# Optimization experiments

Hardware: AMD Instinct MI355X
Metric: run time of the kernel (lower is better)

The kernel has to match this reference:

```python
import jax, jax.numpy as jnp
import numpy as np

N_NODES = 200000
N_EDGES = 2000000
N_GRAPHS = 10000
N_LAYERS = 2
BN_EPS = 1e-5


def setup_inputs() -> dict:
    key = jax.random.key(0)
    ks = jax.random.split(key, 24)
    inp = {
        "x": jax.random.normal(ks[0], (N_NODES, 14), dtype=jnp.float32),
        "edge_index": jax.random.randint(ks[1], (2, N_EDGES), 0, N_NODES, dtype=jnp.int32),
        "edge_attr": jax.random.normal(ks[2], (N_EDGES, 3), dtype=jnp.float32),
        "batch": jnp.sort(jax.random.randint(ks[3], (N_NODES,), 0, N_GRAPHS, dtype=jnp.int32)),
        # embeddings
        "node_w": jax.random.normal(ks[4], (14, 32), dtype=jnp.float32) * 0.2,
        "node_b": jnp.zeros((32,), dtype=jnp.float32),
        "edge_w": jax.random.normal(ks[5], (3, 32), dtype=jnp.float32) * 0.2,
        "edge_b": jnp.zeros((32,), dtype=jnp.float32),
        # per-layer GINE MLP (32->75->32) + BatchNorm params, stacked over layers
        "w1": jax.random.normal(ks[6], (N_LAYERS, 32, 75), dtype=jnp.float32) * 0.15,
        "b1": jnp.zeros((N_LAYERS, 75), dtype=jnp.float32),
        "w2": jax.random.normal(ks[7], (N_LAYERS, 75, 32), dtype=jnp.float32) * 0.15,
        "b2": jnp.zeros((N_LAYERS, 32), dtype=jnp.float32),
        "bn_g": jnp.ones((N_LAYERS, 32), dtype=jnp.float32),
        "bn_b": jnp.zeros((N_LAYERS, 32), dtype=jnp.float32),
        # readout head
        "lin1_w": jax.random.normal(ks[8], (32, 16), dtype=jnp.float32) * 0.2,
        "lin1_b": jnp.zeros((16,), dtype=jnp.float32),
        "lin2_w": jax.random.normal(ks[9], (16, 2), dtype=jnp.float32) * 0.2,
        "lin2_b": jnp.zeros((2,), dtype=jnp.float32),
    }
    return inp


def reference(x, edge_index, edge_attr, batch,
              node_w, node_b, edge_w, edge_b,
              w1, b1, w2, b2, bn_g, bn_b,
              lin1_w, lin1_b, lin2_w, lin2_b):
    n = x.shape[0]
    src, dst = edge_index[0], edge_index[1]
    h = x @ node_w + node_b                      # [N,32]
    e = edge_attr @ edge_w + edge_b              # [E,32]
    for l in range(N_LAYERS):
        # GINEConv: (1+eps)*x + sum_j ReLU(x_j + e_ij), eps=0, then MLP
        msg = jax.nn.relu(h[src] + e)            # [E,32] gather + edge add
        agg = jax.ops.segment_sum(msg, dst, num_segments=n)  # scatter-sum
        z = h + agg
        z = jax.nn.relu(z @ w1[l] + b1[l]) @ w2[l] + b2[l]
        # BatchNorm (training-mode batch statistics, biased var)
        mu = jnp.mean(z, axis=0)
        var = jnp.var(z, axis=0)
        z = (z - mu) * jax.lax.rsqrt(var + BN_EPS) * bn_g[l] + bn_b[l]
        h = jax.nn.relu(z)
    # global mean pool over graphs
    counts = jax.ops.segment_sum(jnp.ones((n,), dtype=h.dtype), batch, num_segments=N_GRAPHS)
    g = jax.ops.segment_sum(h, batch, num_segments=N_GRAPHS) / jnp.maximum(counts, 1.0)[:, None]
    pred = jax.nn.relu(g @ lin1_w + lin1_b) @ lin2_w + lin2_b  # [G,2] logits
    return pred
```

## Files before the change

kernel.cpp:

```cpp
#include <hip/hip_runtime.h>
#include <hip/hip_fp16.h>

#define NN 200000
#define NE 2000000
#define NG 10000

#define NPB 256
#define NBKT 782
#define EPB 8192
#define NPBLK 245
#define SCAN_N (NBKT * NPBLK)
#define SCAN_PAD 191592
#define NSB1 ((SCAN_N + 255) / 256)

typedef __fp16 h2 __attribute__((ext_vector_type(2)));

__device__ __forceinline__ void fadd(float* p, float v) {
    unsafeAtomicAdd(p, v);
}

__device__ __forceinline__ float fdot2(h2 a, h2 b, float c) {
#if __has_builtin(__builtin_amdgcn_fdot2)
    return __builtin_amdgcn_fdot2(a, b, c, false);
#else
    return c + (float)a.x * (float)b.x + (float)a.y * (float)b.y;
#endif
}

__device__ __forceinline__ h2 pk16(float a, float b) {
#if __has_builtin(__builtin_amdgcn_cvt_pkrtz)
    return __builtin_amdgcn_cvt_pkrtz(a, b);
#else
    h2 r;
    r.x = (__fp16)a;
    r.y = (__fp16)b;
    return r;
#endif
}

__device__ __forceinline__ float4 h16_load4(const __half* p) {
    uint2 r = *reinterpret_cast<const uint2*>(p);
    __half2 a = *reinterpret_cast<__half2*>(&r.x);
    __half2 b = *reinterpret_cast<__half2*>(&r.y);
    float2 f0 = __half22float2(a);
    float2 f1 = __half22float2(b);
    return make_float4(f0.x, f0.y, f1.x, f1.y);
}

__device__ __forceinline__ void h16_store4(__half* p, float4 v) {
    __half2 a = __floats2half2_rn(v.x, v.y);
    __half2 b = __floats2half2_rn(v.z, v.w);
    uint2 r;
    r.x = *reinterpret_cast<uint*>(&a);
    r.y = *reinterpret_cast<uint*>(&b);
    *reinterpret_cast<uint2*>(p) = r;
}

__global__ __launch_bounds__(256) void k_node_embed(const float* __restrict__ x,
                                                    const float* __restrict__ w,
                                                    const float* __restrict__ b,
                                                    __half* __restrict__ h16) {
    __shared__ float sw[14 * 32];
    __shared__ float sb[32];
    for (int i = threadIdx.x; i < 14 * 32; i += 256) sw[i] = w[i];
    if (threadIdx.x < 32) sb[threadIdx.x] = b[threadIdx.x];
    __syncthreads();
    int n = blockIdx.x * 256 + threadIdx.x;
    if (n >= NN) return;
    float xi[14];
#pragma unroll
    for (int k = 0; k < 14; ++k) xi[k] = x[n * 14 + k];
#pragma unroll
    for (int c = 0; c < 32; c += 4) {
        float4 acc = make_float4(sb[c], sb[c + 1], sb[c + 2], sb[c + 3]);
#pragma unroll
        for (int k = 0; k < 14; ++k) {
            float xv = xi[k];
            acc.x += xv * sw[k * 32 + c + 0];
            acc.y += xv * sw[k * 32 + c + 1];
            acc.z += xv * sw[k * 32 + c + 2];
            acc.w += xv * sw[k * 32 + c + 3];
        }
        h16_store4(h16 + (size_t)n * 32 + c, acc);
    }
}

__global__ __launch_bounds__(256) void k_prep(const float* __restrict__ w1,
                                              const float* __restrict__ b1,
                                              const float* __restrict__ w2,
                                              uint* __restrict__ w1h,
                                              uint* __restrict__ w2p,
                                              float* __restrict__ b1p) {
    int i = blockIdx.x * 256 + threadIdx.x;
    if (i < 2 * 76 * 16) {
        int l = i / (76 * 16), r = i % (76 * 16);
        int j = r / 16, p = r % 16;
        float a = (j < 75) ? w1[l * 2400 + (2 * p) * 75 + j] : 0.f;
        float b = (j < 75) ? w1[l * 2400 + (2 * p + 1) * 75 + j] : 0.f;
        uint lo = __half_as_ushort(__float2half_rn(a));
        uint hi = __half_as_ushort(__float2half_rn(b));
        w1h[i] = lo | (hi << 16);
        return;
    }
    int i2 = i - 2 * 76 * 16;
    if (i2 >= 0 && i2 < 2 * 38 * 32) {
        int l = i2 / (38 * 32), r = i2 % (38 * 32);
        int jp = r / 32, k = r % 32;
        float a = w2[l * 2400 + (2 * jp) * 32 + k];
        float b = (2 * jp + 1 < 75) ? w2[l * 2400 + (2 * jp + 1) * 32 + k] : 0.f;
        uint lo = __half_as_ushort(__float2half_rn(a));
        uint hi = __half_as_ushort(__float2half_rn(b));
        w2p[i2] = lo | (hi << 16);
        return;
    }
    int i3 = i2 - 2 * 38 * 32;
    if (i3 >= 0 && i3 < 2 * 76) {
        int l = i3 / 76, j = i3 % 76;
        b1p[i3] = (j < 75) ? b1[l * 75 + j] : 0.f;
    }
}

__global__ __launch_bounds__(1024) void k_hist(const int* __restrict__ ei,
                                               int* __restrict__ counts) {
    __shared__ int hist[NBKT];
    for (int i = threadIdx.x; i < NBKT; i += 1024) hist[i] = 0;
    __syncthreads();
    int base = blockIdx.x * EPB;
#pragma unroll
    for (int k = 0; k < EPB / 1024; ++k) {
        int e = base + k * 1024 + threadIdx.x;
        if (e < NE) atomicAdd(&hist[ei[NE + e] >> 8], 1);
    }
    __syncthreads();
    for (int b = threadIdx.x; b < NBKT; b += 1024)
        counts[b * NPBLK + blockIdx.x] = hist[b];
}

__global__ __launch_bounds__(256) void k_scanA(int* __restrict__ data,
                                               int* __restrict__ part) {
    __shared__ int s[256];
    int tid = threadIdx.x;
    int i = blockIdx.x * 256 + tid;
    int v = (i < SCAN_N) ? data[i] : 0;
    s[tid] = v;
    __syncthreads();
    for (int off = 1; off < 256; off <<= 1) {
        int t = (tid >= off) ? s[tid - off] : 0;
        __syncthreads();
        s[tid] += t;
        __syncthreads();
    }
    if (i < SCAN_N) data[i] = s[tid] - v;
    if (tid == 255) part[blockIdx.x] = s[255];
}

__global__ __launch_bounds__(1024) void k_scanB(int* __restrict__ part) {
    __shared__ int s[1024];
    int tid = threadIdx.x;
    int v = (tid < NSB1) ? part[tid] : 0;
    s[tid] = v;
    __syncthreads();
    for (int off = 1; off < 1024; off <<= 1) {
        int t = (tid >= off) ? s[tid - off] : 0;
        __syncthreads();
        s[tid] += t;
        __syncthreads();
    }
    if (tid < NSB1) part[tid] = s[tid] - v;
}

__global__ __launch_bounds__(256) void k_scanC(int* __restrict__ data,
                                               const int* __restrict__ part) {
    int i = blockIdx.x * 256 + threadIdx.x;
    if (i < SCAN_N) data[i] += part[blockIdx.x];
}

__global__ __launch_bounds__(1024) void k_part_scatter(const int* __restrict__ ei,
                                                       const float* __restrict__ ea,
                                                       const int* __restrict__ counts,
                                                       uint3* __restrict__ tmp) {
    __shared__ int sbase[NBKT];
    __shared__ int scnt[NBKT];
    for (int i = threadIdx.x; i < NBKT; i += 1024) {
        sbase[i] = counts[i * NPBLK + blockIdx.x];
        scnt[i] = 0;
    }
    __syncthreads();
    int base = blockIdx.x * EPB;
#pragma unroll
    for (int k = 0; k < EPB / 1024; ++k) {
        int e = base + k * 1024 + threadIdx.x;
        if (e >= NE) continue;
        int dst = ei[NE + e];
        int bkt = dst >> 8;
        int nl = dst & 255;
        int r = atomicAdd(&scnt[bkt], 1);
        int src = ei[e];
        __half2 p01 = __floats2half2_rn(ea[e * 3 + 0], ea[e * 3 + 1]);
        __half p2 = __float2half_rn(ea[e * 3 + 2]);
        uint3 rec;
        rec.x = (uint)(src | (nl << 24));
        rec.y = *reinterpret_cast<const uint*>(&p01);
        rec.z = (uint)__half_as_ushort(p2);
        tmp[sbase[bkt] + r] = rec;
    }
}

__global__ __launch_bounds__(512) void k_bucket_sort(const int* __restrict__ counts,
                                                     const uint3* __restrict__ tmp,
                                                     uint3* __restrict__ recs2,
                                                     int* __restrict__ row_off) {
    __shared__ int cnt[NPB];
    __shared__ int s[NPB];
    int tid = threadIdx.x;
    int b = blockIdx.x;
    int boff = counts[b * NPBLK];
    int bend = (b == NBKT - 1) ? NE : counts[(b + 1) * NPBLK];
    if (tid < NPB) cnt[tid] = 0;
    __syncthreads();
    for (int i = boff + tid; i < bend; i += 512)
        atomicAdd(&cnt[(tmp[i].x >> 24) & 255], 1);
    __syncthreads();
    int v = (tid < NPB) ? cnt[tid] : 0;
    if (tid < NPB) s[tid] = v;
    __syncthreads();
    for (int off = 1; off < 256; off <<= 1) {
        int t = (tid >= off && tid < NPB) ? s[tid - off] : 0;
        __syncthreads();
        if (tid < NPB) s[tid] += t;
        __syncthreads();
    }
    if (tid < NPB) {
        int excl = s[tid] - v;
        int n = b * NPB + tid;
        if (n < NN) row_off[n] = boff + excl;
        cnt[tid] = excl;
    }
    if (b == NBKT - 1 && tid == 0) row_off[NN] = NE;
    __syncthreads();
    for (int i = boff + tid; i < bend; i += 512) {
        uint3 r = tmp[i];
        int nl = (r.x >> 24) & 255;
        int p = atomicAdd(&cnt[nl], 1);
        recs2[boff + p] = r;
    }
}

__global__ __launch_bounds__(256) void k_aggregate(const int* __restrict__ row_off,
                                                   const uint3* __restrict__ recs,
                                                   const float* __restrict__ ew,
                                                   const float* __restrict__ eb,
                                                   const __half* __restrict__ h16,
                                                   float* __restrict__ agg) {
    __shared__ float sw[96];
    __shared__ float sb[32];
    if (threadIdx.x < 96) sw[threadIdx.x] = ew[threadIdx.x];
    if (threadIdx.x < 32) sb[threadIdx.x] = eb[threadIdx.x];
    __syncthreads();
    int t = blockIdx.x * 256 + threadIdx.x;
    int n = t >> 2;
    if (n >= NN) return;
    int c = (t & 3) * 8;
    float w0[8], w1[8], w2[8], bb[8], acc[8];
#pragma unroll
    for (int j = 0; j < 8; ++j) {
        w0[j] = sw[c + j];
        w1[j] = sw[32 + c + j];
        w2[j] = sw[64 + c + j];
        bb[j] = sb[c + j];
        acc[j] = 0.f;
    }
    int s0 = row_off[n], s1 = row_off[n + 1];
    int i = s0;
    for (; i + 2 <= s1; i += 2) {
        uint3 r0 = recs[i];
        uint3 r1 = recs[i + 1];
        int src0 = r0.x & 0x00FFFFFF;
        int src1 = r1.x & 0x00FFFFFF;
        uint4 ha = *(const uint4*)(h16 + (size_t)src0 * 32 + c);
        uint4 hb = *(const uint4*)(h16 + (size_t)src1 * 32 + c);
        float2 e01a = __half22float2(*reinterpret_cast<const __half2*>(&r0.y));
        float e2a = __half2float(__ushort_as_half((unsigned short)(r0.z & 0xFFFF)));
        float2 e01b = __half22float2(*reinterpret_cast<const __half2*>(&r1.y));
        float e2b = __half2float(__ushort_as_half((unsigned short)(r1.z & 0xFFFF)));
        float fa[8], fb[8];
        {
            float2 t0 = __half22float2(*reinterpret_cast<const __half2*>(&ha.x));
            float2 t1 = __half22float2(*reinterpret_cast<const __half2*>(&ha.y));
            float2 t2 = __half22float2(*reinterpret_cast<const __half2*>(&ha.z));
            float2 t3 = __half22float2(*reinterpret_cast<const __half2*>(&ha.w));
            fa[0] = t0.x; fa[1] = t0.y; fa[2] = t1.x; fa[3] = t1.y;
            fa[4] = t2.x; fa[5] = t2.y; fa[6] = t3.x; fa[7] = t3.y;
            float2 u0 = __half22float2(*reinterpret_cast<const __half2*>(&hb.x));
            float2 u1 = __half22float2(*reinterpret_cast<const __half2*>(&hb.y));
            float2 u2 = __half22float2(*reinterpret_cast<const __half2*>(&hb.z));
            float2 u3 = __half22float2(*reinterpret_cast<const __half2*>(&hb.w));
            fb[0] = u0.x; fb[1] = u0.y; fb[2] = u1.x; fb[3] = u1.y;
            fb[4] = u2.x; fb[5] = u2.y; fb[6] = u3.x; fb[7] = u3.y;
        }
#pragma unroll
        for (int j = 0; j < 8; ++j) {
            float ma = fa[j] + bb[j] + e01a.x * w0[j] + e01a.y * w1[j] + e2a * w2[j];
            float mb = fb[j] + bb[j] + e01b.x * w0[j] + e01b.y * w1[j] + e2b * w2[j];
            acc[j] += fmaxf(ma, 0.f) + fmaxf(mb, 0.f);
        }
    }
    if (i < s1) {
        uint3 r0 = recs[i];
        int src0 = r0.x & 0x00FFFFFF;
        uint4 ha = *(const uint4*)(h16 + (size_t)src0 * 32 + c);
        float2 e01a = __half22float2(*reinterpret_cast<const __half2*>(&r0.y));
        float e2a = __half2float(__ushort_as_half((unsigned short)(r0.z & 0xFFFF)));
        float2 t0 = __half22float2(*reinterpret_cast<const __half2*>(&ha.x));
        float2 t1 = __half22float2(*reinterpret_cast<const __half2*>(&ha.y));
        float2 t2 = __half22float2(*reinterpret_cast<const __half2*>(&ha.z));
        float2 t3 = __half22float2(*reinterpret_cast<const __half2*>(&ha.w));
        float fa[8] = {t0.x, t0.y, t1.x, t1.y, t2.x, t2.y, t3.x, t3.y};
#pragma unroll
        for (int j = 0; j < 8; ++j) {
            float ma = fa[j] + bb[j] + e01a.x * w0[j] + e01a.y * w1[j] + e2a * w2[j];
            acc[j] += fmaxf(ma, 0.f);
        }
    }
    *(float4*)(agg + (size_t)n * 32 + c) = make_float4(acc[0], acc[1], acc[2], acc[3]);
    *(float4*)(agg + (size_t)n * 32 + c + 4) = make_float4(acc[4], acc[5], acc[6], acc[7]);
}

__global__ __launch_bounds__(256) void k_edge_scatter(const int* __restrict__ ei,
                                                      const float* __restrict__ ea,
                                                      const float* __restrict__ ew,
                                                      const float* __restrict__ eb,
                                                      const __half* __restrict__ h16,
                                                      float* __restrict__ agg) {
    __shared__ float sw[96];
    __shared__ float sb[32];
    if (threadIdx.x < 96) sw[threadIdx.x] = ew[threadIdx.x];
    if (threadIdx.x < 32) sb[threadIdx.x] = eb[threadIdx.x];
    __syncthreads();
    int t = blockIdx.x * 256 + threadIdx.x;
    int edge = t >> 3;
    if (edge >= NE) return;
    int c = (t & 7) * 4;
    int src = ei[edge];
    int dst = ei[NE + edge];
    float a0 = ea[edge * 3 + 0];
    float a1 = ea[edge * 3 + 1];
    float a2 = ea[edge * 3 + 2];
    float4 hs = h16_load4(h16 + (size_t)src * 32 + c);
    float m0 = hs.x + sb[c + 0] + a0 * sw[c + 0] + a1 * sw[32 + c + 0] + a2 * sw[64 + c + 0];
    float m1 = hs.y + sb[c + 1] + a0 * sw[c + 1] + a1 * sw[32 + c + 1] + a2 * sw[64 + c + 1];
    float m2 = hs.z + sb[c + 2] + a0 * sw[c + 2] + a1 * sw[32 + c + 2] + a2 * sw[64 + c + 2];
    float m3 = hs.w + sb[c + 3] + a0 * sw[c + 3] + a1 * sw[32 + c + 3] + a2 * sw[64 + c + 3];
    float* o = agg + (size_t)dst * 32 + c;
    fadd(o + 0, fmaxf(m0, 0.f));
    fadd(o + 1, fmaxf(m1, 0.f));
    fadd(o + 2, fmaxf(m2, 0.f));
    fadd(o + 3, fmaxf(m3, 0.f));
}

__global__ __launch_bounds__(256) void k_mlp_stats(const __half* __restrict__ h16,
                                                   float* __restrict__ zio,
                                                   const uint* __restrict__ w1h_u,
                                                   const float* __restrict__ b1p,
                                                   const uint* __restrict__ w2p_u,
                                                   const float* __restrict__ b2,
                                                   float* __restrict__ stats) {
    __shared__ float ls[4][64];
    const h2* w1h = reinterpret_cast<const h2*>(w1h_u);
    const h2* w2p = reinterpret_cast<const h2*>(w2p_u);
    int tid = threadIdx.x;
    int n = blockIdx.x * 256 + tid;
    bool valid = n < NN;
    h2 zp[16];
    float acc[32];
    if (valid) {
#pragma unroll
        for (int c = 0; c < 32; c += 4) {
            float4 hv = h16_load4(h16 + (size_t)n * 32 + c);
            float4 av = *(const float4*)(zio + (size_t)n * 32 + c);
            zp[c / 2] = pk16(hv.x + av.x, hv.y + av.y);
            zp[c / 2 + 1] = pk16(hv.z + av.z, hv.w + av.w);
        }
    } else {
#pragma unroll
        for (int p = 0; p < 16; ++p) zp[p] = pk16(0.f, 0.f);
    }
#pragma unroll
    for (int k = 0; k < 32; ++k) acc[k] = b2[k];
    for (int jp = 0; jp < 38; ++jp) {
        float t0 = b1p[2 * jp];
        float t1 = b1p[2 * jp + 1];
        const h2* r0 = w1h + (2 * jp) * 16;
        const h2* r1 = w1h + (2 * jp + 1) * 16;
#pragma unroll
        for (int p = 0; p < 16; ++p) {
            t0 = fdot2(zp[p], r0[p], t0);
            t1 = fdot2(zp[p], r1[p], t1);
        }
        t0 = fmaxf(t0, 0.f);
        t1 = fmaxf(t1, 0.f);
        h2 tp = pk16(t0, t1);
        const h2* c2 = w2p + jp * 32;
#pragma unroll
        for (int k = 0; k < 32; ++k) acc[k] = fdot2(tp, c2[k], acc[k]);
    }
    if (valid) {
#pragma unroll
        for (int c = 0; c < 32; c += 4)
            *(float4*)(zio + (size_t)n * 32 + c) = make_float4(acc[c], acc[c + 1], acc[c + 2], acc[c + 3]);
    } else {
#pragma unroll
        for (int k = 0; k < 32; ++k) acc[k] = 0.f;
    }
    int wave = tid >> 6, lane = tid & 63;
#pragma unroll
    for (int k = 0; k < 32; ++k) {
        float sv = acc[k];
        float qv = sv * sv;
#pragma unroll
        for (int off = 1; off < 64; off <<= 1) {
            sv += __shfl_xor(sv, off);
            qv += __shfl_xor(qv, off);
        }
        if (lane == 0) {
            ls[wave][k] = sv;
            ls[wave][32 + k] = qv;
        }
    }
    __syncthreads();
    if (tid < 64)
        fadd(&stats[tid], ls[0][tid] + ls[1][tid] + ls[2][tid] + ls[3][tid]);
}

__global__ __launch_bounds__(256) void k_norm_relu(const float* __restrict__ z,
                                                   const float* __restrict__ stats,
                                                   const float* __restrict__ g,
                                                   const float* __restrict__ bnb,
                                                   __half* __restrict__ h16) {
    __shared__ float sc[32], sh[32];
    if (threadIdx.x < 32) {
        int cc = threadIdx.x;
        float mu = stats[cc] * (1.0f / NN);
        float var = stats[32 + cc] * (1.0f / NN) - mu * mu;
        float s = g[cc] * rsqrtf(var + 1e-5f);
        sc[cc] = s;
        sh[cc] = bnb[cc] - mu * s;
    }
    __syncthreads();
    int i = blockIdx.x * 256 + threadIdx.x;
    if (i >= NN * 8) return;
    int c = (i & 7) * 4;
    float4 v = *(const float4*)(z + (size_t)i * 4);
    float4 o;
    o.x = fmaxf(v.x * sc[c + 0] + sh[c + 0], 0.f);
    o.y = fmaxf(v.y * sc[c + 1] + sh[c + 1], 0.f);
    o.z = fmaxf(v.z * sc[c + 2] + sh[c + 2], 0.f);
    o.w = fmaxf(v.w * sc[c + 3] + sh[c + 3], 0.f);
    h16_store4(h16 + (size_t)i * 4, o);
}

__global__ __launch_bounds__(256) void k_pool(const __half* __restrict__ h16,
                                              const int* __restrict__ batch,
                                              float* __restrict__ gsum,
                                              float* __restrict__ gcnt) {
    int gid = blockIdx.x * 256 + threadIdx.x;
    int nb = (gid >> 3) * 8;
    if (nb >= NN) return;
    int c = (gid & 7) * 4;
    bool lead = (gid & 7) == 0;
    float4 acc = make_float4(0.f, 0.f, 0.f, 0.f);
    float cnt = 0.f;
    int cur = batch[nb];
#pragma unroll
    for (int k = 0; k < 8; ++k) {
        int n = nb + k;
        if (n >= NN) break;
        int bg = batch[n];
        if (bg != cur) {
            float* o = gsum + (size_t)cur * 32 + c;
            fadd(o + 0, acc.x); fadd(o + 1, acc.y);
            fadd(o + 2, acc.z); fadd(o + 3, acc.w);
            if (lead) fadd(&gcnt[cur], cnt);
            acc = make_float4(0.f, 0.f, 0.f, 0.f);
            cnt = 0.f;
            cur = bg;
        }
        float4 v = h16_load4(h16 + (size_t)n * 32 + c);
        acc.x += v.x; acc.y += v.y; acc.z += v.z; acc.w += v.w;
        cnt += 1.f;
    }
    float* o = gsum + (size_t)cur * 32 + c;
    fadd(o + 0, acc.x); fadd(o + 1, acc.y);
    fadd(o + 2, acc.z); fadd(o + 3, acc.w);
    if (lead) fadd(&gcnt[cur], cnt);
}

__global__ __launch_bounds__(256) void k_head(const float* __restrict__ gsum,
                                              const float* __restrict__ gcnt,
                                              const float* __restrict__ l1w,
                                              const float* __restrict__ l1b,
                                              const float* __restrict__ l2w,
                                              const float* __restrict__ l2b,
                                              float* __restrict__ out) {
    __shared__ float s1[32 * 16], sb1[16], s2[16 * 2], sb2[2];
    for (int i = threadIdx.x; i < 512; i += 256) s1[i] = l1w[i];
    if (threadIdx.x < 16) sb1[threadIdx.x] = l1b[threadIdx.x];
    if (threadIdx.x < 32) s2[threadIdx.x] = l2w[threadIdx.x];
    if (threadIdx.x < 2) sb2[threadIdx.x] = l2b[threadIdx.x];
    __syncthreads();
    int gi = blockIdx.x * 256 + threadIdx.x;
    if (gi >= NG) return;
    float inv = 1.0f / fmaxf(gcnt[gi], 1.0f);
    float gm[32];
#pragma unroll
    for (int c = 0; c < 32; c += 4) {
        float4 v = *(const float4*)(gsum + (size_t)gi * 32 + c);
        gm[c + 0] = v.x * inv;
        gm[c + 1] = v.y * inv;
        gm[c + 2] = v.z * inv;
        gm[c + 3] = v.w * inv;
    }
    float a[16];
#pragma unroll
    for (int j = 0; j < 16; ++j) {
        float t = sb1[j];
#pragma unroll
        for (int c = 0; c < 32; ++c) t += gm[c] * s1[c * 16 + j];
        a[j] = fmaxf(t, 0.f);
    }
    float o0 = sb2[0], o1 = sb2[1];
#pragma unroll
    for (int j = 0; j < 16; ++j) {
        o0 += a[j] * s2[j * 2 + 0];
        o1 += a[j] * s2[j * 2 + 1];
    }
    out[gi * 2 + 0] = o0;
    out[gi * 2 + 1] = o1;
}

extern "C" void kernel_launch(void* const* d_in, const int* in_sizes, int n_in,
                              void* d_out, int out_size, void* d_ws, size_t ws_size,
                              hipStream_t stream) {
    const float* x = (const float*)d_in[0];
    const int* ei = (const int*)d_in[1];
    const float* ea = (const float*)d_in[2];
    const int* batch = (const int*)d_in[3];
    const float* node_w = (const float*)d_in[4];
    const float* node_b = (const float*)d_in[5];
    const float* edge_w = (const float*)d_in[6];
    const float* edge_b = (const float*)d_in[7];
    const float* w1 = (const float*)d_in[8];
    const float* b1 = (const float*)d_in[9];
    const float* w2 = (const float*)d_in[10];
    const float* b2 = (const float*)d_in[11];
    const float* bng = (const float*)d_in[12];
    const float* bnb = (const float*)d_in[13];
    const float* l1w = (const float*)d_in[14];
    const float* l1b = (const float*)d_in[15];
    const float* l2w = (const float*)d_in[16];
    const float* l2b = (const float*)d_in[17];
    float* out = (float*)d_out;

    float* base = (float*)d_ws;
    __half* h16 = (__half*)base;
    float* zb = base + 3200000;
    float* gsum = zb + (size_t)NN * 32;
    float* gcnt = gsum + (size_t)NG * 32;
    float* stats = gcnt + NG;
    uint* w1h = (uint*)(stats + 64);
    uint* w2p = w1h + 2 * 76 * 16;
    float* b1p = (float*)(w2p + 2 * 38 * 32);
    int* counts = (int*)(b1p + 152);
    int* part = counts + SCAN_PAD;
    int* row_off = part + 1024;
    uint3* recs2 = (uint3*)(row_off + NN + 4);
    uint3* tmp = (uint3*)zb;

    size_t need_f = 3200000 + (size_t)NN * 32 + (size_t)NG * 33 + 64 + 2432 + 2432 + 152 +
                    SCAN_PAD + 1024 + ((size_t)NN + 4) + (size_t)NE * 3;
    bool use_fast = ws_size >= need_f * 4;

    if (use_fast) {
        k_hist<<<NPBLK, 1024, 0, stream>>>(ei, counts);
        k_scanA<<<NSB1, 256, 0, stream>>>(counts, part);
        k_scanB<<<1, 1024, 0, stream>>>(part);
        k_scanC<<<NSB1, 256, 0, stream>>>(counts, part);
        k_part_scatter<<<NPBLK, 1024, 0, stream>>>(ei, ea, counts, tmp);
        k_bucket_sort<<<NBKT, 512, 0, stream>>>(counts, tmp, recs2, row_off);
    }
    k_prep<<<(2 * 76 * 16 + 2 * 38 * 32 + 2 * 76 + 255) / 256, 256, 0, stream>>>(
        w1, b1, w2, w1h, w2p, b1p);

    k_node_embed<<<(NN + 255) / 256, 256, 0, stream>>>(x, node_w, node_b, h16);

    for (int l = 0; l < 2; ++l) {
        (void)hipMemsetAsync(stats, 0, 64 * sizeof(float), stream);
        if (use_fast) {
            k_aggregate<<<(NN * 4 + 255) / 256, 256, 0, stream>>>(row_off, recs2,
                                                                  edge_w, edge_b, h16, zb);
        } else {
            (void)hipMemsetAsync(zb, 0, (size_t)NN * 32 * sizeof(float), stream);
            k_edge_scatter<<<(NE * 8) / 256, 256, 0, stream>>>(ei, ea, edge_w, edge_b, h16, zb);
        }
        k_mlp_stats<<<(NN + 255) / 256, 256, 0, stream>>>(h16, zb, w1h + l * 76 * 16,
                                                          b1p + l * 76, w2p + l * 38 * 32,
                                                          b2 + l * 32, stats);
        k_norm_relu<<<(NN * 8 + 255) / 256, 256, 0, stream>>>(zb, stats, bng + l * 32,
                                                              bnb + l * 32, h16);
    }

    (void)hipMemsetAsync(gsum, 0, (size_t)(NG * 33) * sizeof(float), stream);
    k_pool<<<(NN + 255) / 256, 256, 0, stream>>>(h16, batch, gsum, gcnt);
    k_head<<<(NG + 255) / 256, 256, 0, stream>>>(gsum, gcnt, l1w, l1b, l2w, l2b, out);
}
```

Before: 318.1 us.

## Fold BatchNorm+ReLU into consumer kernels and drop the separate normalize pass

Removes the k_norm_relu kernel. The MLP kernel now writes pre-normalization z back into the fp16 node buffer, and the next layer's aggregate/scatter, MLP residual and pooling kernels apply the per-channel scale/shift and ReLU on the fly from the previous layer's stats. Per-layer stats are kept in separate slots, cleared by a single memset. This removes a full fp32 read and fp16 write pass over node features per layer and halves the MLP output store. In exchange, the BN affine is recomputed on every gathered edge, and storing pre-BN values in fp16 adds some precision risk. The first-layer dot products are also split into two accumulators for more instruction-level parallelism.

```diff
diff --git a/kernel.cpp b/kernel.cpp
--- a/kernel.cpp
+++ b/kernel.cpp
@@ -48,8 +48,8 @@
 }
 
 __device__ __forceinline__ void h16_store4(__half* p, float4 v) {
-    __half2 a = __floats2half2_rn(v.x, v.y);
-    __half2 b = __floats2half2_rn(v.z, v.w);
+    h2 a = pk16(v.x, v.y);
+    h2 b = pk16(v.z, v.w);
     uint2 r;
     r.x = *reinterpret_cast<uint*>(&a);
     r.y = *reinterpret_cast<uint*>(&b);
@@ -246,28 +246,53 @@
     }
 }
 
+__device__ __forceinline__ void bn_preamble(float* ssc, float* ssh, int apply,
+                                            const float* in_stats,
+                                            const float* in_g, const float* in_b) {
+    if (threadIdx.x < 32) {
+        float s = 1.f, t = 0.f;
+        if (apply) {
+            int cc = threadIdx.x;
+            float mu = in_stats[cc] * (1.0f / NN);
+            float var = in_stats[32 + cc] * (1.0f / NN) - mu * mu;
+            s = in_g[cc] * rsqrtf(var + 1e-5f);
+            t = in_b[cc] - mu * s;
+        }
+        ssc[threadIdx.x] = s;
+        ssh[threadIdx.x] = t;
+    }
+}
+
 __global__ __launch_bounds__(256) void k_aggregate(const int* __restrict__ row_off,
                                                    const uint3* __restrict__ recs,
                                                    const float* __restrict__ ew,
                                                    const float* __restrict__ eb,
                                                    const __half* __restrict__ h16,
+                                                   const float* __restrict__ in_stats,
+                                                   const float* __restrict__ in_g,
+                                                   const float* __restrict__ in_b,
+                                                   int apply,
                                                    float* __restrict__ agg) {
     __shared__ float sw[96];
     __shared__ float sb[32];
+    __shared__ float ssc[32], ssh[32];
     if (threadIdx.x < 96) sw[threadIdx.x] = ew[threadIdx.x];
     if (threadIdx.x < 32) sb[threadIdx.x] = eb[threadIdx.x];
+    bn_preamble(ssc, ssh, apply, in_stats, in_g, in_b);
     __syncthreads();
     int t = blockIdx.x * 256 + threadIdx.x;
     int n = t >> 2;
     if (n >= NN) return;
     int c = (t & 3) * 8;
-    float w0[8], w1[8], w2[8], bb[8], acc[8];
+    float w0[8], w1[8], w2[8], bb[8], acc[8], sc8[8], sh8[8];
 #pragma unroll
     for (int j = 0; j < 8; ++j) {
         w0[j] = sw[c + j];
         w1[j] = sw[32 + c + j];
         w2[j] = sw[64 + c + j];
         bb[j] = sb[c + j];
+        sc8[j] = ssc[c + j];
+        sh8[j] = ssh[c + j];
         acc[j] = 0.f;
     }
     int s0 = row_off[n], s1 = row_off[n + 1];
@@ -300,8 +325,13 @@
         }
 #pragma unroll
         for (int j = 0; j < 8; ++j) {
-            float ma = fa[j] + bb[j] + e01a.x * w0[j] + e01a.y * w1[j] + e2a * w2[j];
-            float mb = fb[j] + bb[j] + e01b.x * w0[j] + e01b.y * w1[j] + e2b * w2[j];
+            float va = fa[j], vb = fb[j];
+            if (apply) {
+                va = fmaxf(va * sc8[j] + sh8[j], 0.f);
+                vb = fmaxf(vb * sc8[j] + sh8[j], 0.f);
+            }
+            float ma = va + bb[j] + e01a.x * w0[j] + e01a.y * w1[j] + e2a * w2[j];
+            float mb = vb + bb[j] + e01b.x * w0[j] + e01b.y * w1[j] + e2b * w2[j];
             acc[j] += fmaxf(ma, 0.f) + fmaxf(mb, 0.f);
         }
     }
@@ -318,7 +348,9 @@
         float fa[8] = {t0.x, t0.y, t1.x, t1.y, t2.x, t2.y, t3.x, t3.y};
 #pragma unroll
         for (int j = 0; j < 8; ++j) {
-            float ma = fa[j] + bb[j] + e01a.x * w0[j] + e01a.y * w1[j] + e2a * w2[j];
+            float va = fa[j];
+            if (apply) va = fmaxf(va * sc8[j] + sh8[j], 0.f);
+            float ma = va + bb[j] + e01a.x * w0[j] + e01a.y * w1[j] + e2a * w2[j];
             acc[j] += fmaxf(ma, 0.f);
         }
     }
@@ -331,11 +363,17 @@
                                                       const float* __restrict__ ew,
                                                       const float* __restrict__ eb,
                                                       const __half* __restrict__ h16,
+                                                      const float* __restrict__ in_stats,
+                                                      const float* __restrict__ in_g,
+                                                      const float* __restrict__ in_b,
+                                                      int apply,
                                                       float* __restrict__ agg) {
     __shared__ float sw[96];
     __shared__ float sb[32];
+    __shared__ float ssc[32], ssh[32];
     if (threadIdx.x < 96) sw[threadIdx.x] = ew[threadIdx.x];
     if (threadIdx.x < 32) sb[threadIdx.x] = eb[threadIdx.x];
+    bn_preamble(ssc, ssh, apply, in_stats, in_g, in_b);
     __syncthreads();
     int t = blockIdx.x * 256 + threadIdx.x;
     int edge = t >> 3;
@@ -347,6 +385,12 @@
     float a1 = ea[edge * 3 + 1];
     float a2 = ea[edge * 3 + 2];
     float4 hs = h16_load4(h16 + (size_t)src * 32 + c);
+    if (apply) {
+        hs.x = fmaxf(hs.x * ssc[c + 0] + ssh[c + 0], 0.f);
+        hs.y = fmaxf(hs.y * ssc[c + 1] + ssh[c + 1], 0.f);
+        hs.z = fmaxf(hs.z * ssc[c + 2] + ssh[c + 2], 0.f);
+        hs.w = fmaxf(hs.w * ssc[c + 3] + ssh[c + 3], 0.f);
+    }
     float m0 = hs.x + sb[c + 0] + a0 * sw[c + 0] + a1 * sw[32 + c + 0] + a2 * sw[64 + c + 0];
     float m1 = hs.y + sb[c + 1] + a0 * sw[c + 1] + a1 * sw[32 + c + 1] + a2 * sw[64 + c + 1];
     float m2 = hs.z + sb[c + 2] + a0 * sw[c + 2] + a1 * sw[32 + c + 2] + a2 * sw[64 + c + 2];
@@ -358,14 +402,21 @@
     fadd(o + 3, fmaxf(m3, 0.f));
 }
 
-__global__ __launch_bounds__(256) void k_mlp_stats(const __half* __restrict__ h16,
-                                                   float* __restrict__ zio,
+__global__ __launch_bounds__(256) void k_mlp_stats(__half* __restrict__ hio,
+                                                   const float* __restrict__ agg,
                                                    const uint* __restrict__ w1h_u,
                                                    const float* __restrict__ b1p,
                                                    const uint* __restrict__ w2p_u,
                                                    const float* __restrict__ b2,
+                                                   const float* __restrict__ in_stats,
+                                                   const float* __restrict__ in_g,
+                                                   const float* __restrict__ in_b,
+                                                   int apply,
                                                    float* __restrict__ stats) {
     __shared__ float ls[4][64];
+    __shared__ float ssc[32], ssh[32];
+    bn_preamble(ssc, ssh, apply, in_stats, in_g, in_b);
+    __syncthreads();
     const h2* w1h = reinterpret_cast<const h2*>(w1h_u);
     const h2* w2p = reinterpret_cast<const h2*>(w2p_u);
     int tid = threadIdx.x;
@@ -376,8 +427,14 @@
     if (valid) {
 #pragma unroll
         for (int c = 0; c < 32; c += 4) {
-            float4 hv = h16_load4(h16 + (size_t)n * 32 + c);
-            float4 av = *(const float4*)(zio + (size_t)n * 32 + c);
+            float4 hv = h16_load4(hio + (size_t)n * 32 + c);
+            if (apply) {
+                hv.x = fmaxf(hv.x * ssc[c + 0] + ssh[c + 0], 0.f);
+                hv.y = fmaxf(hv.y * ssc[c + 1] + ssh[c + 1], 0.f);
+                hv.z = fmaxf(hv.z * ssc[c + 2] + ssh[c + 2], 0.f);
+                hv.w = fmaxf(hv.w * ssc[c + 3] + ssh[c + 3], 0.f);
+            }
+            float4 av = *(const float4*)(agg + (size_t)n * 32 + c);
             zp[c / 2] = pk16(hv.x + av.x, hv.y + av.y);
             zp[c / 2 + 1] = pk16(hv.z + av.z, hv.w + av.w);
         }
@@ -388,17 +445,19 @@
 #pragma unroll
     for (int k = 0; k < 32; ++k) acc[k] = b2[k];
     for (int jp = 0; jp < 38; ++jp) {
-        float t0 = b1p[2 * jp];
-        float t1 = b1p[2 * jp + 1];
+        float t0a = b1p[2 * jp], t0b = 0.f;
+        float t1a = b1p[2 * jp + 1], t1b = 0.f;
         const h2* r0 = w1h + (2 * jp) * 16;
         const h2* r1 = w1h + (2 * jp + 1) * 16;
 #pragma unroll
-        for (int p = 0; p < 16; ++p) {
-            t0 = fdot2(zp[p], r0[p], t0);
-            t1 = fdot2(zp[p], r1[p], t1);
-        }
-        t0 = fmaxf(t0, 0.f);
-        t1 = fmaxf(t1, 0.f);
+        for (int p = 0; p < 8; ++p) {
+            t0a = fdot2(zp[2 * p], r0[2 * p], t0a);
+            t0b = fdot2(zp[2 * p + 1], r0[2 * p + 1], t0b);
+            t1a = fdot2(zp[2 * p], r1[2 * p], t1a);
+            t1b = fdot2(zp[2 * p + 1], r1[2 * p + 1], t1b);
+        }
+        float t0 = fmaxf(t0a + t0b, 0.f);
+        float t1 = fmaxf(t1a + t1b, 0.f);
         h2 tp = pk16(t0, t1);
         const h2* c2 = w2p + jp * 32;
 #pragma unroll
@@ -407,7 +466,8 @@
     if (valid) {
 #pragma unroll
         for (int c = 0; c < 32; c += 4)
-            *(float4*)(zio + (size_t)n * 32 + c) = make_float4(acc[c], acc[c + 1], acc[c + 2], acc[c + 3]);
+            h16_store4(hio + (size_t)n * 32 + c,
+                       make_float4(acc[c], acc[c + 1], acc[c + 2], acc[c + 3]));
     } else {
 #pragma unroll
         for (int k = 0; k < 32; ++k) acc[k] = 0.f;
@@ -432,42 +492,23 @@
         fadd(&stats[tid], ls[0][tid] + ls[1][tid] + ls[2][tid] + ls[3][tid]);
 }
 
-__global__ __launch_bounds__(256) void k_norm_relu(const float* __restrict__ z,
-                                                   const float* __restrict__ stats,
-                                                   const float* __restrict__ g,
-                                                   const float* __restrict__ bnb,
-                                                   __half* __restrict__ h16) {
-    __shared__ float sc[32], sh[32];
-    if (threadIdx.x < 32) {
-        int cc = threadIdx.x;
-        float mu = stats[cc] * (1.0f / NN);
-        float var = stats[32 + cc] * (1.0f / NN) - mu * mu;
-        float s = g[cc] * rsqrtf(var + 1e-5f);
-        sc[cc] = s;
-        sh[cc] = bnb[cc] - mu * s;
-    }
-    __syncthreads();
-    int i = blockIdx.x * 256 + threadIdx.x;
-    if (i >= NN * 8) return;
-    int c = (i & 7) * 4;
-    float4 v = *(const float4*)(z + (size_t)i * 4);
-    float4 o;
-    o.x = fmaxf(v.x * sc[c + 0] + sh[c + 0], 0.f);
-    o.y = fmaxf(v.y * sc[c + 1] + sh[c + 1], 0.f);
-    o.z = fmaxf(v.z * sc[c + 2] + sh[c + 2], 0.f);
-    o.w = fmaxf(v.w * sc[c + 3] + sh[c + 3], 0.f);
-    h16_store4(h16 + (size_t)i * 4, o);
-}
-
 __global__ __launch_bounds__(256) void k_pool(const __half* __restrict__ h16,
                                               const int* __restrict__ batch,
+                                              const float* __restrict__ in_stats,
+                                              const float* __restrict__ in_g,
+                                              const float* __restrict__ in_b,
                                               float* __restrict__ gsum,
                                               float* __restrict__ gcnt) {
+    __shared__ float ssc[32], ssh[32];
+    bn_preamble(ssc, ssh, 1, in_stats, in_g, in_b);
+    __syncthreads();
     int gid = blockIdx.x * 256 + threadIdx.x;
     int nb = (gid >> 3) * 8;
     if (nb >= NN) return;
     int c = (gid & 7) * 4;
     bool lead = (gid & 7) == 0;
+    float sc0 = ssc[c], sc1 = ssc[c + 1], sc2 = ssc[c + 2], sc3 = ssc[c + 3];
+    float sh0 = ssh[c], sh1 = ssh[c + 1], sh2 = ssh[c + 2], sh3 = ssh[c + 3];
     float4 acc = make_float4(0.f, 0.f, 0.f, 0.f);
     float cnt = 0.f;
     int cur = batch[nb];
@@ -486,7 +527,10 @@
             cur = bg;
         }
         float4 v = h16_load4(h16 + (size_t)n * 32 + c);
-        acc.x += v.x; acc.y += v.y; acc.z += v.z; acc.w += v.w;
+        acc.x += fmaxf(v.x * sc0 + sh0, 0.f);
+        acc.y += fmaxf(v.y * sc1 + sh1, 0.f);
+        acc.z += fmaxf(v.z * sc2 + sh2, 0.f);
+        acc.w += fmaxf(v.w * sc3 + sh3, 0.f);
         cnt += 1.f;
     }
     float* o = gsum + (size_t)cur * 32 + c;
@@ -567,7 +611,7 @@
     float* gsum = zb + (size_t)NN * 32;
     float* gcnt = gsum + (size_t)NG * 32;
     float* stats = gcnt + NG;
-    uint* w1h = (uint*)(stats + 64);
+    uint* w1h = (uint*)(stats + 128);
     uint* w2p = w1h + 2 * 76 * 16;
     float* b1p = (float*)(w2p + 2 * 38 * 32);
     int* counts = (int*)(b1p + 152);
@@ -576,7 +620,7 @@
     uint3* recs2 = (uint3*)(row_off + NN + 4);
     uint3* tmp = (uint3*)zb;
 
-    size_t need_f = 3200000 + (size_t)NN * 32 + (size_t)NG * 33 + 64 + 2432 + 2432 + 152 +
+    size_t need_f = 3200000 + (size_t)NN * 32 + (size_t)NG * 33 + 128 + 2432 + 2432 + 152 +
                     SCAN_PAD + 1024 + ((size_t)NN + 4) + (size_t)NE * 3;
     bool use_fast = ws_size >= need_f * 4;
 
@@ -593,23 +637,35 @@
 
     k_node_embed<<<(NN + 255) / 256, 256, 0, stream>>>(x, node_w, node_b, h16);
 
+    (void)hipMemsetAsync(stats, 0, 128 * sizeof(float), stream);
+
     for (int l = 0; l < 2; ++l) {
-        (void)hipMemsetAsync(stats, 0, 64 * sizeof(float), stream);
+        const float* pst = (l == 0) ? stats : stats;
+        const float* ist = (l == 0) ? stats : stats + 0;
+        const float* ig = bng + (l - 1) * 32;
+        const float* ib = bnb + (l - 1) * 32;
+        int apply = (l > 0) ? 1 : 0;
+        const float* prev_stats = (l > 0) ? (stats + (l - 1) * 64) : stats;
+        (void)pst; (void)ist;
+        if (l == 0) { ig = bng; ib = bnb; }
         if (use_fast) {
             k_aggregate<<<(NN * 4 + 255) / 256, 256, 0, stream>>>(row_off, recs2,
-                                                                  edge_w, edge_b, h16, zb);
+                                                                  edge_w, edge_b, h16,
+                                                                  prev_stats, ig, ib, apply, zb);
         } else {
             (void)hipMemsetAsync(zb, 0, (size_t)NN * 32 * sizeof(float), stream);
-            k_edge_scatter<<<(NE * 8) / 256, 256, 0, stream>>>(ei, ea, edge_w, edge_b, h16, zb);
+            k_edge_scatter<<<(NE * 8) / 256, 256, 0, stream>>>(ei, ea, edge_w, edge_b, h16,
+                                                               prev_stats, ig, ib, apply, zb);
         }
         k_mlp_stats<<<(NN + 255) / 256, 256, 0, stream>>>(h16, zb, w1h + l * 76 * 16,
                                                           b1p + l * 76, w2p + l * 38 * 32,
-                                                          b2 + l * 32, stats);
-        k_norm_relu<<<(NN * 8 + 255) / 256, 256, 0, stream>>>(zb, stats, bng + l * 32,
-                                                              bnb + l * 32, h16);
+                                                          b2 + l * 32,
+                                                          prev_stats, ig, ib, apply,
+                                                          stats + l * 64);
     }
 
     (void)hipMemsetAsync(gsum, 0, (size_t)(NG * 33) * sizeof(float), stream);
-    k_pool<<<(NN + 255) / 256, 256, 0, stream>>>(h16, batch, gsum, gcnt);
+    k_pool<<<(NN + 255) / 256, 256, 0, stream>>>(h16, batch, stats + 64, bng + 32, bnb + 32,
+                                                 gsum, gcnt);
     k_head<<<(NG + 255) / 256, 256, 0, stream>>>(gsum, gcnt, l1w, l1b, l2w, l2b, out);
 }
```

New measurement: 329.9 us. 3.7% more time.
